# Kernel tuning notes

Hardware: AMD Instinct MI355X
Metric: run time of the kernel (lower is better)

Reference implementation:

```python
import jax, jax.numpy as jnp
import numpy as np

N = 100000      # nodes
E = 1600000     # directed edges (avg degree 16)
F_IN = 128
HID = 64
OUT = 10


def setup_inputs() -> dict:
    key = jax.random.key(0)
    ks = jax.random.split(key, 6)
    x = jax.random.normal(ks[0], (N, F_IN), dtype=jnp.float32)
    edge_index = jax.random.randint(ks[1], (2, E), 0, N, dtype=jnp.int32)
    # Glorot-scaled weights like PyG's GCNConv.lin; bias added post-aggregation
    W1 = jax.random.normal(ks[2], (F_IN, HID), dtype=jnp.float32) * np.float32(1.0 / np.sqrt(F_IN))
    b1 = jnp.zeros((HID,), dtype=jnp.float32)
    W2 = jax.random.normal(ks[3], (HID, OUT), dtype=jnp.float32) * np.float32(1.0 / np.sqrt(HID))
    b2 = jnp.zeros((OUT,), dtype=jnp.float32)
    return {"x": x, "edge_index": edge_index, "W1": W1, "b1": b1, "W2": W2, "b2": b2}


def _gcn_norm(edge_index, num_nodes):
    """Add self-loops and compute symmetric normalization D^-1/2 A D^-1/2 (PyG gcn_norm)."""
    loops = jnp.arange(num_nodes, dtype=edge_index.dtype)
    src = jnp.concatenate([edge_index[0], loops])
    dst = jnp.concatenate([edge_index[1], loops])
    deg = jax.ops.segment_sum(jnp.ones_like(dst, dtype=jnp.float32), dst, num_segments=num_nodes)
    dinv = jnp.where(deg > 0, jax.lax.rsqrt(deg), 0.0)  # inf -> 0 as in PyG
    norm = dinv[src] * dinv[dst]  # [E+N]
    return src, dst, norm


def _gcn_conv(x, src, dst, norm, W, b, num_nodes):
    h = x @ W                                   # transform first (smaller dim aggregated)
    msg = h[src] * norm[:, None]                # gather + scale
    agg = jax.ops.segment_sum(msg, dst, num_segments=num_nodes)  # scatter-add
    return agg + b


def reference(x, edge_index, W1, b1, W2, b2):
    src, dst, norm = _gcn_norm(edge_index, N)
    h = jax.nn.relu(_gcn_conv(x, src, dst, norm, W1, b1, N))
    # F.dropout(training=self.training): identity in eval mode
    out = _gcn_conv(h, src, dst, norm, W2, b2, N)
    return out
```

## Files before the change

### kernel.cpp

```cpp
#include <hip/hip_runtime.h>
#include <hip/hip_fp16.h>

static constexpr int F = 128;
static constexpr int H = 64;
static constexpr int O = 10;
static constexpr int PSU = 6;
static constexpr int NBUK_MAX = 256;
static constexpr int CAP = 12288;
static constexpr int ESCAP = 14336;
static constexpr int EPB = 4096;
static constexpr int XPAD = 136;

typedef _Float16 half8 __attribute__((ext_vector_type(8)));
typedef float floatx4 __attribute__((ext_vector_type(4)));

__global__ __launch_bounds__(256) void k_init(int* __restrict__ bcntg,
                                              const float* __restrict__ W1,
                                              __half* __restrict__ W1f,
                                              unsigned* __restrict__ yN,
                                              unsigned* __restrict__ zsN) {
    int b = blockIdx.x, t = threadIdx.x;
    if (b == 0) {
        bcntg[t] = 0;
        if (t < 32) yN[t] = 0u;
        if (t < PSU) zsN[t] = 0u;
    } else {
        int i = (b - 1) * 256 + t;
        int j = i & 7, lane = (i >> 3) & 63, sc = i >> 9;
        int s = sc >> 2, c = sc & 3;
        int k = s * 32 + (lane >> 4) * 8 + j;
        int nn = c * 16 + (lane & 15);
        W1f[i] = __float2half(W1[k * H + nn]);
    }
}

__global__ __launch_bounds__(256) void k_bin(const int* __restrict__ src,
                                             const int* __restrict__ dst,
                                             int* __restrict__ bcntg,
                                             unsigned* __restrict__ ebuf, int e_total) {
    __shared__ int hist[NBUK_MAX];
    __shared__ int base[NBUK_MAX];
    __shared__ int loc[NBUK_MAX];
    int t = threadIdx.x;
    hist[t] = 0;
    loc[t] = 0;
    __syncthreads();
    int i0 = blockIdx.x * EPB;
    int i1 = min(i0 + EPB, e_total);
    int i = i0 + 4 * t;
    for (; i + 3 < i1; i += 1024) {
        int4 d4 = *(const int4*)&dst[i];
        atomicAdd(&hist[d4.x >> 9], 1);
        atomicAdd(&hist[d4.y >> 9], 1);
        atomicAdd(&hist[d4.z >> 9], 1);
        atomicAdd(&hist[d4.w >> 9], 1);
    }
    for (; i < i1; ++i) atomicAdd(&hist[dst[i] >> 9], 1);
    __syncthreads();
    if (hist[t] > 0) base[t] = atomicAdd(&bcntg[t], hist[t]);
    __syncthreads();
    i = i0 + 4 * t;
    for (; i + 3 < i1; i += 1024) {
        int4 s4 = *(const int4*)&src[i];
        int4 d4 = *(const int4*)&dst[i];
#pragma unroll
        for (int u = 0; u < 4; ++u) {
            int s = (&s4.x)[u], d = (&d4.x)[u];
            int b = d >> 9;
            int r = base[b] + atomicAdd(&loc[b], 1);
            if (r < CAP)
                ebuf[(size_t)b * CAP + r] = ((unsigned)(d & 511) << 17) | (unsigned)s;
        }
    }
    for (; i < i1; ++i) {
        int s = src[i], d = dst[i];
        int b = d >> 9;
        int r = base[b] + atomicAdd(&loc[b], 1);
        if (r < CAP)
            ebuf[(size_t)b * CAP + r] = ((unsigned)(d & 511) << 17) | (unsigned)s;
    }
}

__global__ __launch_bounds__(256) void k_bsort(
    const unsigned* __restrict__ ebuf, const int* __restrict__ bcntg,
    int* __restrict__ rowbeg, int* __restrict__ degp, float* __restrict__ dinv,
    int* __restrict__ esrc, int n_nodes) {
    __shared__ int hc[512];
    __shared__ int sa[512];
    __shared__ int sb[512];
    int t = threadIdx.x, b = blockIdx.x, n0 = b << 9;
    hc[t] = 0;
    hc[t + 256] = 0;
    __syncthreads();
    int cb = min(bcntg[b], CAP);
    const unsigned* eb = ebuf + (size_t)b * CAP;
    int i = 4 * t;
    for (; i + 3 < cb; i += 1024) {
        uint4 e4 = *(const uint4*)&eb[i];
        atomicAdd(&hc[e4.x >> 17], 1);
        atomicAdd(&hc[e4.y >> 17], 1);
        atomicAdd(&hc[e4.z >> 17], 1);
        atomicAdd(&hc[e4.w >> 17], 1);
    }
    for (; i < cb; ++i) atomicAdd(&hc[eb[i] >> 17], 1);
    __syncthreads();
#pragma unroll
    for (int u = 0; u < 2; ++u) {
        int ii = t + 256 * u;
        sa[ii] = (hc[ii] + 7) & ~7;
    }
    __syncthreads();
    int* A = sa;
    int* Bp = sb;
    for (int off = 1; off < 512; off <<= 1) {
#pragma unroll
        for (int u = 0; u < 2; ++u) {
            int ii = t + 256 * u;
            int v = A[ii];
            if (ii >= off) v += A[ii - off];
            Bp[ii] = v;
        }
        __syncthreads();
        int* tmp = A; A = Bp; Bp = tmp;
    }
#pragma unroll
    for (int u = 0; u < 2; ++u) {
        int ii = t + 256 * u;
        int cnt = hc[ii];
        int cp = (cnt + 7) & ~7;
        int excl = A[ii] - cp;
        Bp[ii] = excl;
        int n = n0 + ii;
        if (n < n_nodes) {
            rowbeg[n] = b * ESCAP + excl;
            degp[n] = cp;
            dinv[n] = rsqrtf((float)cnt + 1.0f);
        }
    }
    __syncthreads();
    int* es = esrc + (size_t)b * ESCAP;
    i = 4 * t;
    for (; i + 3 < cb; i += 1024) {
        uint4 e4 = *(const uint4*)&eb[i];
#pragma unroll
        for (int u = 0; u < 4; ++u) {
            unsigned e = (&e4.x)[u];
            int r = atomicAdd(&Bp[e >> 17], 1);
            es[r] = (int)(e & 0x1FFFFu);
        }
    }
    for (; i < cb; ++i) {
        unsigned e = eb[i];
        int r = atomicAdd(&Bp[e >> 17], 1);
        es[r] = (int)(e & 0x1FFFFu);
    }
    __syncthreads();
#pragma unroll
    for (int u = 0; u < 2; ++u) {
        int ii = t + 256 * u;
        int end = A[ii];
        for (int p = Bp[ii]; p < end; ++p) es[p] = n_nodes;
    }
}

__global__ __launch_bounds__(256, 4) void k_gemm1(
    const float* __restrict__ x, const __half* __restrict__ W1f,
    const float* __restrict__ dinv, __half* __restrict__ y, int n_nodes) {
    __shared__ __half xh[64 * XPAD];
    const int tid = threadIdx.x;
    const int lane = tid & 63;
    const int w = tid >> 6;
    const int row0 = blockIdx.x * 64;

    half8 bf[16];
    const uint4* wf = (const uint4*)W1f;
#pragma unroll
    for (int sc = 0; sc < 16; ++sc) {
        union { uint4 u; half8 h; } tmp;
        tmp.u = wf[sc * 64 + lane];
        bf[sc] = tmp.h;
    }

    for (int i = tid; i < 64 * 32; i += 256) {
        int r = i >> 5, k4 = i & 31;
        int gr = row0 + r;
        if (gr < n_nodes) {
            float4 v = *(const float4*)&x[(size_t)gr * F + 4 * k4];
            __half2 p0 = __floats2half2_rn(v.x, v.y);
            __half2 p1 = __floats2half2_rn(v.z, v.w);
            uint2 pk = make_uint2(*(unsigned*)&p0, *(unsigned*)&p1);
            *(uint2*)&xh[r * XPAD + 4 * k4] = pk;
        }
    }
    __syncthreads();

    const int m16 = lane & 15, quad = lane >> 4;
    floatx4 acc[4];
#pragma unroll
    for (int c = 0; c < 4; ++c) acc[c] = (floatx4){0.f, 0.f, 0.f, 0.f};
#pragma unroll
    for (int s = 0; s < 4; ++s) {
        union { uint4 u; half8 h; } ua;
        ua.u = *(const uint4*)&xh[(16 * w + m16) * XPAD + s * 32 + quad * 8];
#pragma unroll
        for (int c = 0; c < 4; ++c)
            acc[c] = __builtin_amdgcn_mfma_f32_16x16x32_f16(ua.h, bf[s * 4 + c],
                                                            acc[c], 0, 0, 0);
    }
#pragma unroll
    for (int r = 0; r < 4; ++r) {
        int grow = row0 + 16 * w + quad * 4 + r;
        if (grow < n_nodes) {
            float d = dinv[grow];
#pragma unroll
            for (int c = 0; c < 4; ++c)
                y[(size_t)grow * H + c * 16 + m16] = __float2half(acc[c][r] * d);
        }
    }
}

__global__ __launch_bounds__(256) void k_gather1z(
    const uint4* __restrict__ yq4, const int* __restrict__ rowbeg,
    const int* __restrict__ degp, const int* __restrict__ esrc,
    const float* __restrict__ dinv, const float* __restrict__ b1,
    const float* __restrict__ W2, unsigned* __restrict__ zs_u, int n_nodes) {
    __shared__ float w2t[O * H];
    for (int i = threadIdx.x; i < O * H; i += 256)
        w2t[i] = W2[(i & 63) * O + (i >> 6)];
    __syncthreads();
    const int l = threadIdx.x & 63;
    const int c = l & 7;
    const int gbase = l & ~7;
    const int n = blockIdx.x * 32 + (threadIdx.x >> 3);
    if (n >= n_nodes) return;
    const int beg = rowbeg[n];
    const int dp = degp[n];
    const float d = dinv[n];

    float acc[8];
    {
        uint4 v = yq4[(size_t)n * 8 + c];
        float2 f0 = __half22float2(*(const __half2*)&v.x);
        float2 f1 = __half22float2(*(const __half2*)&v.y);
        float2 f2 = __half22float2(*(const __half2*)&v.z);
        float2 f3 = __half22float2(*(const __half2*)&v.w);
        acc[0] = f0.x; acc[1] = f0.y; acc[2] = f1.x; acc[3] = f1.y;
        acc[4] = f2.x; acc[5] = f2.y; acc[6] = f3.x; acc[7] = f3.y;
    }
    for (int k0 = 0; k0 < dp; k0 += 8) {
        int idx = esrc[beg + k0 + c];
#pragma unroll
        for (int e = 0; e < 8; ++e) {
            int s = __shfl(idx, gbase + e, 64);
            uint4 v = yq4[(size_t)s * 8 + c];
            float2 f0 = __half22float2(*(const __half2*)&v.x);
            float2 f1 = __half22float2(*(const __half2*)&v.y);
            float2 f2 = __half22float2(*(const __half2*)&v.z);
            float2 f3 = __half22float2(*(const __half2*)&v.w);
            acc[0] += f0.x; acc[1] += f0.y; acc[2] += f1.x; acc[3] += f1.y;
            acc[4] += f2.x; acc[5] += f2.y; acc[6] += f3.x; acc[7] += f3.y;
        }
    }
    const float4 ba = ((const float4*)b1)[2 * c];
    const float4 bbv = ((const float4*)b1)[2 * c + 1];
    float h[8];
    h[0] = fmaxf(fmaf(d, acc[0], ba.x), 0.0f);
    h[1] = fmaxf(fmaf(d, acc[1], ba.y), 0.0f);
    h[2] = fmaxf(fmaf(d, acc[2], ba.z), 0.0f);
    h[3] = fmaxf(fmaf(d, acc[3], ba.w), 0.0f);
    h[4] = fmaxf(fmaf(d, acc[4], bbv.x), 0.0f);
    h[5] = fmaxf(fmaf(d, acc[5], bbv.y), 0.0f);
    h[6] = fmaxf(fmaf(d, acc[6], bbv.z), 0.0f);
    h[7] = fmaxf(fmaf(d, acc[7], bbv.w), 0.0f);
    float p[O];
#pragma unroll
    for (int j = 0; j < O; ++j) {
        float4 wa = *(const float4*)&w2t[j * 64 + 8 * c];
        float4 wb = *(const float4*)&w2t[j * 64 + 8 * c + 4];
        p[j] = h[0] * wa.x + h[1] * wa.y + h[2] * wa.z + h[3] * wa.w
             + h[4] * wb.x + h[5] * wb.y + h[6] * wb.z + h[7] * wb.w;
    }
#pragma unroll
    for (int m = 1; m <= 4; m <<= 1) {
#pragma unroll
        for (int j = 0; j < O; ++j) p[j] += __shfl_xor(p[j], m, 64);
    }
    if (c == 0) {
        __half2 q0 = __floats2half2_rn(p[0] * d, p[1] * d);
        __half2 q1 = __floats2half2_rn(p[2] * d, p[3] * d);
        __half2 q2 = __floats2half2_rn(p[4] * d, p[5] * d);
        __half2 q3 = __floats2half2_rn(p[6] * d, p[7] * d);
        __half2 q4 = __floats2half2_rn(p[8] * d, p[9] * d);
        uint2* zp = (uint2*)&zs_u[(size_t)n * PSU];
        zp[0] = make_uint2(*(const unsigned*)&q0, *(const unsigned*)&q1);
        zp[1] = make_uint2(*(const unsigned*)&q2, *(const unsigned*)&q3);
        zp[2] = make_uint2(*(const unsigned*)&q4, 0u);
    }
}

__global__ __launch_bounds__(256) void k_gather2(
    const unsigned* __restrict__ zs_u, const int* __restrict__ rowbeg,
    const int* __restrict__ degp, const int* __restrict__ esrc,
    const float* __restrict__ dinv, const float* __restrict__ b2,
    float* __restrict__ out, int n_nodes) {
    const int l = threadIdx.x & 63;
    const int j = l & 3;
    const int gb = l & ~3;
    const int jj = (j < 3) ? j : 2;
    const int n = blockIdx.x * 64 + (threadIdx.x >> 2);
    if (n >= n_nodes) return;
    const int beg = rowbeg[n];
    const int dp = degp[n];
    uint2 v0 = *(const uint2*)&zs_u[(size_t)n * PSU + 2 * jj];
    float2 accA = __half22float2(*(const __half2*)&v0.x);
    float2 accB = __half22float2(*(const __half2*)&v0.y);
    for (int k0 = 0; k0 < dp; k0 += 8) {
        int2 idx = *(const int2*)&esrc[beg + k0 + 2 * j];
#pragma unroll
        for (int e = 0; e < 8; ++e) {
            int s = __shfl((e & 1) ? idx.y : idx.x, gb + (e >> 1), 64);
            uint2 v = *(const uint2*)&zs_u[(size_t)s * PSU + 2 * jj];
            float2 fA = __half22float2(*(const __half2*)&v.x);
            float2 fB = __half22float2(*(const __half2*)&v.y);
            accA.x += fA.x; accA.y += fA.y;
            accB.x += fB.x; accB.y += fB.y;
        }
    }
    if (j < 3) {
        const float d = dinv[n];
        float2 bbA = ((const float2*)b2)[2 * j];
        float2 oA = make_float2(fmaf(d, accA.x, bbA.x), fmaf(d, accA.y, bbA.y));
        *(float2*)&out[(size_t)n * O + 4 * j] = oA;
        if (j < 2) {
            float2 bbB = ((const float2*)b2)[2 * j + 1];
            float2 oB = make_float2(fmaf(d, accB.x, bbB.x), fmaf(d, accB.y, bbB.y));
            *(float2*)&out[(size_t)n * O + 4 * j + 2] = oB;
        }
    }
}

static inline size_t align256(size_t v) { return (v + 255) & ~(size_t)255; }

extern "C" void kernel_launch(void* const* d_in, const int* in_sizes, int n_in,
                              void* d_out, int out_size, void* d_ws, size_t ws_size,
                              hipStream_t stream) {
    const float* x  = (const float*)d_in[0];
    const int*   ei = (const int*)d_in[1];
    const float* W1 = (const float*)d_in[2];
    const float* b1 = (const float*)d_in[3];
    const float* W2 = (const float*)d_in[4];
    const float* b2 = (const float*)d_in[5];
    float* out = (float*)d_out;

    const int N = in_sizes[0] / F;
    const int E = in_sizes[1] / 2;
    const int* src = ei;
    const int* dst = ei + E;
    const int NBUK = (N + 511) >> 9;

    char* base = (char*)d_ws;
    __half* y = (__half*)base;
    size_t ysz = align256((size_t)(N + 1) * H * 2);
    char* hreg = base + ysz;
    unsigned* ebuf = (unsigned*)hreg;
    __half* W1f = (__half*)(hreg + (size_t)N * H * 2 - (size_t)F * H * 2);
    size_t hsz = align256((size_t)N * H * 2);
    char* zreg = hreg + hsz;
    unsigned* zs_u = (unsigned*)zreg;
    size_t zsz = align256((size_t)(N + 1) * PSU * 4);
    float* dinv = (float*)(zreg + zsz);
    int* rowbeg = (int*)(dinv + N);
    int* degp = rowbeg + N;
    int* bcntg = degp + N;
    int* esrc = bcntg + 256;

    const int nb_bin = (E + EPB - 1) / EPB;

    k_init<<<1 + F * H / 256, 256, 0, stream>>>(bcntg, W1, W1f,
                                                (unsigned*)(y + (size_t)N * H),
                                                zs_u + (size_t)N * PSU);
    k_bin<<<nb_bin, 256, 0, stream>>>(src, dst, bcntg, ebuf, E);
    k_bsort<<<NBUK, 256, 0, stream>>>(ebuf, bcntg, rowbeg, degp, dinv, esrc, N);
    k_gemm1<<<(N + 63) / 64, 256, 0, stream>>>(x, W1f, dinv, y, N);
    k_gather1z<<<(N + 31) / 32, 256, 0, stream>>>((const uint4*)y, rowbeg, degp,
                                                  esrc, dinv, b1, W2, zs_u, N);
    k_gather2<<<(N + 63) / 64, 256, 0, stream>>>(zs_u, rowbeg, degp, esrc,
                                                 dinv, b2, out, N);
}
```

Baseline: 189.7 us.

## Replace bucket sort CSR build with global degree atomics and fuse scatter into GEMM launch

The two-pass bucketed CSR construction (bin into per-bucket buffers, then a per-bucket local sort) is replaced with a global-atomic degree count, a per-bucket scan that writes row starts and cursors, and a scatter pass using global atomics on per-node cursors. The scatter blocks are merged into the same launch as the first GEMM, so edge scattering and the feature transform can run concurrently and one launch plus the intermediate ebuf traffic go away. In exchange, every edge now does a global atomic to a random node address, which may contend more than the previous LDS atomics. Edge order within each row also becomes nondeterministic.

```diff
diff --git a/kernel.cpp b/kernel.cpp
--- a/kernel.cpp
+++ b/kernel.cpp
@@ -5,8 +5,6 @@
 static constexpr int H = 64;
 static constexpr int O = 10;
 static constexpr int PSU = 6;
-static constexpr int NBUK_MAX = 256;
-static constexpr int CAP = 12288;
 static constexpr int ESCAP = 14336;
 static constexpr int EPB = 4096;
 static constexpr int XPAD = 136;
@@ -14,18 +12,21 @@
 typedef _Float16 half8 __attribute__((ext_vector_type(8)));
 typedef float floatx4 __attribute__((ext_vector_type(4)));
 
-__global__ __launch_bounds__(256) void k_init(int* __restrict__ bcntg,
+__global__ __launch_bounds__(256) void k_init(int* __restrict__ deg,
                                               const float* __restrict__ W1,
                                               __half* __restrict__ W1f,
                                               unsigned* __restrict__ yN,
-                                              unsigned* __restrict__ zsN) {
+                                              unsigned* __restrict__ zsN,
+                                              int n_nodes) {
     int b = blockIdx.x, t = threadIdx.x;
-    if (b == 0) {
-        bcntg[t] = 0;
+    if (b < 391) {
+        int i = b * 256 + t;
+        if (i < n_nodes) deg[i] = 0;
+    } else if (b == 391) {
         if (t < 32) yN[t] = 0u;
         if (t < PSU) zsN[t] = 0u;
     } else {
-        int i = (b - 1) * 256 + t;
+        int i = (b - 392) * 256 + t;
         int j = i & 7, lane = (i >> 3) & 63, sc = i >> 9;
         int s = sc >> 2, c = sc & 3;
         int k = s * 32 + (lane >> 4) * 8 + j;
@@ -34,80 +35,36 @@
     }
 }
 
-__global__ __launch_bounds__(256) void k_bin(const int* __restrict__ src,
-                                             const int* __restrict__ dst,
-                                             int* __restrict__ bcntg,
-                                             unsigned* __restrict__ ebuf, int e_total) {
-    __shared__ int hist[NBUK_MAX];
-    __shared__ int base[NBUK_MAX];
-    __shared__ int loc[NBUK_MAX];
-    int t = threadIdx.x;
-    hist[t] = 0;
-    loc[t] = 0;
-    __syncthreads();
-    int i0 = blockIdx.x * EPB;
-    int i1 = min(i0 + EPB, e_total);
-    int i = i0 + 4 * t;
-    for (; i + 3 < i1; i += 1024) {
+__global__ __launch_bounds__(256) void k_deg(const int* __restrict__ dst,
+                                             int* __restrict__ deg, int e_total) {
+    int i = (blockIdx.x * 256 + threadIdx.x) * 4;
+    if (i + 3 < e_total) {
         int4 d4 = *(const int4*)&dst[i];
-        atomicAdd(&hist[d4.x >> 9], 1);
-        atomicAdd(&hist[d4.y >> 9], 1);
-        atomicAdd(&hist[d4.z >> 9], 1);
-        atomicAdd(&hist[d4.w >> 9], 1);
-    }
-    for (; i < i1; ++i) atomicAdd(&hist[dst[i] >> 9], 1);
-    __syncthreads();
-    if (hist[t] > 0) base[t] = atomicAdd(&bcntg[t], hist[t]);
-    __syncthreads();
-    i = i0 + 4 * t;
-    for (; i + 3 < i1; i += 1024) {
-        int4 s4 = *(const int4*)&src[i];
-        int4 d4 = *(const int4*)&dst[i];
-#pragma unroll
-        for (int u = 0; u < 4; ++u) {
-            int s = (&s4.x)[u], d = (&d4.x)[u];
-            int b = d >> 9;
-            int r = base[b] + atomicAdd(&loc[b], 1);
-            if (r < CAP)
-                ebuf[(size_t)b * CAP + r] = ((unsigned)(d & 511) << 17) | (unsigned)s;
-        }
-    }
-    for (; i < i1; ++i) {
-        int s = src[i], d = dst[i];
-        int b = d >> 9;
-        int r = base[b] + atomicAdd(&loc[b], 1);
-        if (r < CAP)
-            ebuf[(size_t)b * CAP + r] = ((unsigned)(d & 511) << 17) | (unsigned)s;
-    }
-}
-
-__global__ __launch_bounds__(256) void k_bsort(
-    const unsigned* __restrict__ ebuf, const int* __restrict__ bcntg,
-    int* __restrict__ rowbeg, int* __restrict__ degp, float* __restrict__ dinv,
-    int* __restrict__ esrc, int n_nodes) {
-    __shared__ int hc[512];
+        atomicAdd(&deg[d4.x], 1);
+        atomicAdd(&deg[d4.y], 1);
+        atomicAdd(&deg[d4.z], 1);
+        atomicAdd(&deg[d4.w], 1);
+    } else {
+        for (; i < e_total; ++i) atomicAdd(&deg[dst[i]], 1);
+    }
+}
+
+__global__ __launch_bounds__(256) void k_scan(
+    const int* __restrict__ deg, int* __restrict__ rowbeg, int* __restrict__ degp,
+    float* __restrict__ dinv, int* __restrict__ wcur, int* __restrict__ esrc,
+    int n_nodes) {
     __shared__ int sa[512];
     __shared__ int sb[512];
     int t = threadIdx.x, b = blockIdx.x, n0 = b << 9;
-    hc[t] = 0;
-    hc[t + 256] = 0;
-    __syncthreads();
-    int cb = min(bcntg[b], CAP);
-    const unsigned* eb = ebuf + (size_t)b * CAP;
-    int i = 4 * t;
-    for (; i + 3 < cb; i += 1024) {
-        uint4 e4 = *(const uint4*)&eb[i];
-        atomicAdd(&hc[e4.x >> 17], 1);
-        atomicAdd(&hc[e4.y >> 17], 1);
-        atomicAdd(&hc[e4.z >> 17], 1);
-        atomicAdd(&hc[e4.w >> 17], 1);
-    }
-    for (; i < cb; ++i) atomicAdd(&hc[eb[i] >> 17], 1);
-    __syncthreads();
+    int cnt[2], cp[2];
 #pragma unroll
     for (int u = 0; u < 2; ++u) {
         int ii = t + 256 * u;
-        sa[ii] = (hc[ii] + 7) & ~7;
+        int n = n0 + ii;
+        int c = (n < n_nodes) ? deg[n] : 0;
+        cnt[u] = c;
+        cp[u] = (c + 7) & ~7;
+        sa[ii] = cp[u];
     }
     __syncthreads();
     int* A = sa;
@@ -126,51 +83,51 @@
 #pragma unroll
     for (int u = 0; u < 2; ++u) {
         int ii = t + 256 * u;
-        int cnt = hc[ii];
-        int cp = (cnt + 7) & ~7;
-        int excl = A[ii] - cp;
-        Bp[ii] = excl;
         int n = n0 + ii;
         if (n < n_nodes) {
-            rowbeg[n] = b * ESCAP + excl;
-            degp[n] = cp;
-            dinv[n] = rsqrtf((float)cnt + 1.0f);
-        }
-    }
-    __syncthreads();
-    int* es = esrc + (size_t)b * ESCAP;
-    i = 4 * t;
-    for (; i + 3 < cb; i += 1024) {
-        uint4 e4 = *(const uint4*)&eb[i];
-#pragma unroll
-        for (int u = 0; u < 4; ++u) {
-            unsigned e = (&e4.x)[u];
-            int r = atomicAdd(&Bp[e >> 17], 1);
-            es[r] = (int)(e & 0x1FFFFu);
-        }
-    }
-    for (; i < cb; ++i) {
-        unsigned e = eb[i];
-        int r = atomicAdd(&Bp[e >> 17], 1);
-        es[r] = (int)(e & 0x1FFFFu);
-    }
-    __syncthreads();
-#pragma unroll
-    for (int u = 0; u < 2; ++u) {
-        int ii = t + 256 * u;
-        int end = A[ii];
-        for (int p = Bp[ii]; p < end; ++p) es[p] = n_nodes;
-    }
-}
-
-__global__ __launch_bounds__(256, 4) void k_gemm1(
+            int excl = A[ii] - cp[u];
+            int beg = b * ESCAP + excl;
+            rowbeg[n] = beg;
+            degp[n] = cp[u];
+            dinv[n] = rsqrtf((float)cnt[u] + 1.0f);
+            wcur[n] = beg;
+            for (int p = beg + cnt[u]; p < beg + cp[u]; ++p)
+                esrc[p] = n_nodes;
+        }
+    }
+}
+
+__global__ __launch_bounds__(256, 4) void k_scatter_gemm(
+    const int* __restrict__ src, const int* __restrict__ dst,
+    int* __restrict__ wcur, int* __restrict__ esrc,
     const float* __restrict__ x, const __half* __restrict__ W1f,
-    const float* __restrict__ dinv, __half* __restrict__ y, int n_nodes) {
+    const float* __restrict__ dinv, __half* __restrict__ y,
+    int n_nodes, int e_total, int nb_sc) {
     __shared__ __half xh[64 * XPAD];
     const int tid = threadIdx.x;
+    if ((int)blockIdx.x < nb_sc) {
+        int i0 = blockIdx.x * EPB;
+        int i1 = min(i0 + EPB, e_total);
+        int i = i0 + 4 * tid;
+        for (; i + 3 < i1; i += 1024) {
+            int4 s4 = *(const int4*)&src[i];
+            int4 d4 = *(const int4*)&dst[i];
+#pragma unroll
+            for (int u = 0; u < 4; ++u) {
+                int s = (&s4.x)[u], d = (&d4.x)[u];
+                int r = atomicAdd(&wcur[d], 1);
+                esrc[r] = s;
+            }
+        }
+        for (; i < i1; ++i) {
+            int r = atomicAdd(&wcur[dst[i]], 1);
+            esrc[r] = src[i];
+        }
+        return;
+    }
     const int lane = tid & 63;
     const int w = tid >> 6;
-    const int row0 = blockIdx.x * 64;
+    const int row0 = ((int)blockIdx.x - nb_sc) * 64;
 
     half8 bf[16];
     const uint4* wf = (const uint4*)W1f;
@@ -362,7 +319,8 @@
     __half* y = (__half*)base;
     size_t ysz = align256((size_t)(N + 1) * H * 2);
     char* hreg = base + ysz;
-    unsigned* ebuf = (unsigned*)hreg;
+    int* deg = (int*)hreg;
+    int* wcur = deg + N;
     __half* W1f = (__half*)(hreg + (size_t)N * H * 2 - (size_t)F * H * 2);
     size_t hsz = align256((size_t)N * H * 2);
     char* zreg = hreg + hsz;
@@ -371,17 +329,18 @@
     float* dinv = (float*)(zreg + zsz);
     int* rowbeg = (int*)(dinv + N);
     int* degp = rowbeg + N;
-    int* bcntg = degp + N;
-    int* esrc = bcntg + 256;
-
-    const int nb_bin = (E + EPB - 1) / EPB;
-
-    k_init<<<1 + F * H / 256, 256, 0, stream>>>(bcntg, W1, W1f,
-                                                (unsigned*)(y + (size_t)N * H),
-                                                zs_u + (size_t)N * PSU);
-    k_bin<<<nb_bin, 256, 0, stream>>>(src, dst, bcntg, ebuf, E);
-    k_bsort<<<NBUK, 256, 0, stream>>>(ebuf, bcntg, rowbeg, degp, dinv, esrc, N);
-    k_gemm1<<<(N + 63) / 64, 256, 0, stream>>>(x, W1f, dinv, y, N);
+    int* esrc = degp + N;
+
+    const int NB_SC = (E + EPB - 1) / EPB;
+    const int NB_GM = (N + 63) / 64;
+
+    k_init<<<392 + F * H / 256, 256, 0, stream>>>(deg, W1, W1f,
+                                                  (unsigned*)(y + (size_t)N * H),
+                                                  zs_u + (size_t)N * PSU, N);
+    k_deg<<<(E + 1023) / 1024, 256, 0, stream>>>(dst, deg, E);
+    k_scan<<<NBUK, 256, 0, stream>>>(deg, rowbeg, degp, dinv, wcur, esrc, N);
+    k_scatter_gemm<<<NB_SC + NB_GM, 256, 0, stream>>>(src, dst, wcur, esrc,
+                                                      x, W1f, dinv, y, N, E, NB_SC);
     k_gather1z<<<(N + 31) / 32, 256, 0, stream>>>((const uint4*)y, rowbeg, degp,
                                                   esrc, dinv, b1, W2, zs_u, N);
     k_gather2<<<(N + 63) / 64, 256, 0, stream>>>(zs_u, rowbeg, degp, esrc,
```

Measured after the change: 299.3 us. 57.7% more time.

## Compute degrees in binning pass and fuse bucket sort with layer-1 GEMM

Applied to the files above, without the earlier changes.

Per-node in-degree is now counted with global atomics during the binning kernel, so the bucket-sort kernel no longer rebuilds a per-bucket histogram from the edge buffer. The bucket sort and the first GEMM become one launch that splits work by block index, and the GEMM computes its normalization from the degree array directly. This removes one kernel launch and the dependency of the GEMM on the sort, letting them overlap. In exchange it adds 1.6M global atomics in k_bin and a zeroing pass in k_init with a hardcoded block count of 391.

```diff
diff --git a/kernel.cpp b/kernel.cpp
--- a/kernel.cpp
+++ b/kernel.cpp
@@ -14,18 +14,23 @@
 typedef _Float16 half8 __attribute__((ext_vector_type(8)));
 typedef float floatx4 __attribute__((ext_vector_type(4)));
 
-__global__ __launch_bounds__(256) void k_init(int* __restrict__ bcntg,
+__global__ __launch_bounds__(256) void k_init(int* __restrict__ deg,
+                                              int* __restrict__ bcntg,
                                               const float* __restrict__ W1,
                                               __half* __restrict__ W1f,
                                               unsigned* __restrict__ yN,
-                                              unsigned* __restrict__ zsN) {
+                                              unsigned* __restrict__ zsN,
+                                              int n_nodes) {
     int b = blockIdx.x, t = threadIdx.x;
-    if (b == 0) {
+    if (b < 391) {
+        int i = b * 256 + t;
+        if (i < n_nodes) deg[i] = 0;
+    } else if (b == 391) {
         bcntg[t] = 0;
         if (t < 32) yN[t] = 0u;
         if (t < PSU) zsN[t] = 0u;
     } else {
-        int i = (b - 1) * 256 + t;
+        int i = (b - 392) * 256 + t;
         int j = i & 7, lane = (i >> 3) & 63, sc = i >> 9;
         int s = sc >> 2, c = sc & 3;
         int k = s * 32 + (lane >> 4) * 8 + j;
@@ -37,6 +42,7 @@
 __global__ __launch_bounds__(256) void k_bin(const int* __restrict__ src,
                                              const int* __restrict__ dst,
                                              int* __restrict__ bcntg,
+                                             int* __restrict__ deg,
                                              unsigned* __restrict__ ebuf, int e_total) {
     __shared__ int hist[NBUK_MAX];
     __shared__ int base[NBUK_MAX];
@@ -54,8 +60,16 @@
         atomicAdd(&hist[d4.y >> 9], 1);
         atomicAdd(&hist[d4.z >> 9], 1);
         atomicAdd(&hist[d4.w >> 9], 1);
-    }
-    for (; i < i1; ++i) atomicAdd(&hist[dst[i] >> 9], 1);
+        atomicAdd(&deg[d4.x], 1);
+        atomicAdd(&deg[d4.y], 1);
+        atomicAdd(&deg[d4.z], 1);
+        atomicAdd(&deg[d4.w], 1);
+    }
+    for (; i < i1; ++i) {
+        int d = dst[i];
+        atomicAdd(&hist[d >> 9], 1);
+        atomicAdd(&deg[d], 1);
+    }
     __syncthreads();
     if (hist[t] > 0) base[t] = atomicAdd(&bcntg[t], hist[t]);
     __syncthreads();
@@ -81,96 +95,85 @@
     }
 }
 
-__global__ __launch_bounds__(256) void k_bsort(
+__global__ __launch_bounds__(256, 4) void k_bsg(
     const unsigned* __restrict__ ebuf, const int* __restrict__ bcntg,
-    int* __restrict__ rowbeg, int* __restrict__ degp, float* __restrict__ dinv,
-    int* __restrict__ esrc, int n_nodes) {
-    __shared__ int hc[512];
+    const int* __restrict__ deg, int* __restrict__ rowbeg, int* __restrict__ degp,
+    float* __restrict__ dinv, int* __restrict__ esrc,
+    const float* __restrict__ x, const __half* __restrict__ W1f,
+    __half* __restrict__ y, int n_nodes, int nb_bs) {
+    __shared__ __half xh[64 * XPAD];
     __shared__ int sa[512];
     __shared__ int sb[512];
-    int t = threadIdx.x, b = blockIdx.x, n0 = b << 9;
-    hc[t] = 0;
-    hc[t + 256] = 0;
-    __syncthreads();
-    int cb = min(bcntg[b], CAP);
-    const unsigned* eb = ebuf + (size_t)b * CAP;
-    int i = 4 * t;
-    for (; i + 3 < cb; i += 1024) {
-        uint4 e4 = *(const uint4*)&eb[i];
-        atomicAdd(&hc[e4.x >> 17], 1);
-        atomicAdd(&hc[e4.y >> 17], 1);
-        atomicAdd(&hc[e4.z >> 17], 1);
-        atomicAdd(&hc[e4.w >> 17], 1);
-    }
-    for (; i < cb; ++i) atomicAdd(&hc[eb[i] >> 17], 1);
-    __syncthreads();
-#pragma unroll
-    for (int u = 0; u < 2; ++u) {
-        int ii = t + 256 * u;
-        sa[ii] = (hc[ii] + 7) & ~7;
-    }
-    __syncthreads();
-    int* A = sa;
-    int* Bp = sb;
-    for (int off = 1; off < 512; off <<= 1) {
+    const int tid = threadIdx.x;
+    if ((int)blockIdx.x < nb_bs) {
+        const int b = blockIdx.x, n0 = b << 9;
+        int cnt[2], cp[2];
 #pragma unroll
         for (int u = 0; u < 2; ++u) {
-            int ii = t + 256 * u;
-            int v = A[ii];
-            if (ii >= off) v += A[ii - off];
-            Bp[ii] = v;
+            int ii = tid + 256 * u;
+            int n = n0 + ii;
+            int c = (n < n_nodes) ? deg[n] : 0;
+            cnt[u] = c;
+            cp[u] = (c + 7) & ~7;
+            sa[ii] = cp[u];
         }
         __syncthreads();
-        int* tmp = A; A = Bp; Bp = tmp;
-    }
-#pragma unroll
-    for (int u = 0; u < 2; ++u) {
-        int ii = t + 256 * u;
-        int cnt = hc[ii];
-        int cp = (cnt + 7) & ~7;
-        int excl = A[ii] - cp;
-        Bp[ii] = excl;
-        int n = n0 + ii;
-        if (n < n_nodes) {
-            rowbeg[n] = b * ESCAP + excl;
-            degp[n] = cp;
-            dinv[n] = rsqrtf((float)cnt + 1.0f);
-        }
-    }
-    __syncthreads();
-    int* es = esrc + (size_t)b * ESCAP;
-    i = 4 * t;
-    for (; i + 3 < cb; i += 1024) {
-        uint4 e4 = *(const uint4*)&eb[i];
-#pragma unroll
-        for (int u = 0; u < 4; ++u) {
-            unsigned e = (&e4.x)[u];
+        int* A = sa;
+        int* Bp = sb;
+        for (int off = 1; off < 512; off <<= 1) {
+#pragma unroll
+            for (int u = 0; u < 2; ++u) {
+                int ii = tid + 256 * u;
+                int v = A[ii];
+                if (ii >= off) v += A[ii - off];
+                Bp[ii] = v;
+            }
+            __syncthreads();
+            int* tmp = A; A = Bp; Bp = tmp;
+        }
+#pragma unroll
+        for (int u = 0; u < 2; ++u) {
+            int ii = tid + 256 * u;
+            int excl = A[ii] - cp[u];
+            Bp[ii] = excl;
+            int n = n0 + ii;
+            if (n < n_nodes) {
+                rowbeg[n] = b * ESCAP + excl;
+                degp[n] = cp[u];
+                dinv[n] = rsqrtf((float)cnt[u] + 1.0f);
+            }
+        }
+        __syncthreads();
+        const int cb = min(bcntg[b], CAP);
+        const unsigned* eb = ebuf + (size_t)b * CAP;
+        int* es = esrc + (size_t)b * ESCAP;
+        int i = 4 * tid;
+        for (; i + 3 < cb; i += 1024) {
+            uint4 e4 = *(const uint4*)&eb[i];
+#pragma unroll
+            for (int u = 0; u < 4; ++u) {
+                unsigned e = (&e4.x)[u];
+                int r = atomicAdd(&Bp[e >> 17], 1);
+                es[r] = (int)(e & 0x1FFFFu);
+            }
+        }
+        for (; i < cb; ++i) {
+            unsigned e = eb[i];
             int r = atomicAdd(&Bp[e >> 17], 1);
             es[r] = (int)(e & 0x1FFFFu);
         }
-    }
-    for (; i < cb; ++i) {
-        unsigned e = eb[i];
-        int r = atomicAdd(&Bp[e >> 17], 1);
-        es[r] = (int)(e & 0x1FFFFu);
-    }
-    __syncthreads();
-#pragma unroll
-    for (int u = 0; u < 2; ++u) {
-        int ii = t + 256 * u;
-        int end = A[ii];
-        for (int p = Bp[ii]; p < end; ++p) es[p] = n_nodes;
-    }
-}
-
-__global__ __launch_bounds__(256, 4) void k_gemm1(
-    const float* __restrict__ x, const __half* __restrict__ W1f,
-    const float* __restrict__ dinv, __half* __restrict__ y, int n_nodes) {
-    __shared__ __half xh[64 * XPAD];
-    const int tid = threadIdx.x;
+        __syncthreads();
+#pragma unroll
+        for (int u = 0; u < 2; ++u) {
+            int ii = tid + 256 * u;
+            int end = A[ii];
+            for (int p = Bp[ii]; p < end; ++p) es[p] = n_nodes;
+        }
+        return;
+    }
     const int lane = tid & 63;
     const int w = tid >> 6;
-    const int row0 = blockIdx.x * 64;
+    const int row0 = ((int)blockIdx.x - nb_bs) * 64;
 
     half8 bf[16];
     const uint4* wf = (const uint4*)W1f;
@@ -211,7 +214,7 @@
     for (int r = 0; r < 4; ++r) {
         int grow = row0 + 16 * w + quad * 4 + r;
         if (grow < n_nodes) {
-            float d = dinv[grow];
+            float d = rsqrtf((float)deg[grow] + 1.0f);
 #pragma unroll
             for (int c = 0; c < 4; ++c)
                 y[(size_t)grow * H + c * 16 + m16] = __float2half(acc[c][r] * d);
@@ -363,6 +366,7 @@
     size_t ysz = align256((size_t)(N + 1) * H * 2);
     char* hreg = base + ysz;
     unsigned* ebuf = (unsigned*)hreg;
+    int* deg = (int*)(hreg + (size_t)NBUK * CAP * 4);
     __half* W1f = (__half*)(hreg + (size_t)N * H * 2 - (size_t)F * H * 2);
     size_t hsz = align256((size_t)N * H * 2);
     char* zreg = hreg + hsz;
@@ -375,13 +379,14 @@
     int* esrc = bcntg + 256;
 
     const int nb_bin = (E + EPB - 1) / EPB;
-
-    k_init<<<1 + F * H / 256, 256, 0, stream>>>(bcntg, W1, W1f,
-                                                (unsigned*)(y + (size_t)N * H),
-                                                zs_u + (size_t)N * PSU);
-    k_bin<<<nb_bin, 256, 0, stream>>>(src, dst, bcntg, ebuf, E);
-    k_bsort<<<NBUK, 256, 0, stream>>>(ebuf, bcntg, rowbeg, degp, dinv, esrc, N);
-    k_gemm1<<<(N + 63) / 64, 256, 0, stream>>>(x, W1f, dinv, y, N);
+    const int NB_GM = (N + 63) / 64;
+
+    k_init<<<392 + F * H / 256, 256, 0, stream>>>(deg, bcntg, W1, W1f,
+                                                  (unsigned*)(y + (size_t)N * H),
+                                                  zs_u + (size_t)N * PSU, N);
+    k_bin<<<nb_bin, 256, 0, stream>>>(src, dst, bcntg, deg, ebuf, E);
+    k_bsg<<<NBUK + NB_GM, 256, 0, stream>>>(ebuf, bcntg, deg, rowbeg, degp,
+                                            dinv, esrc, x, W1f, y, N, NBUK);
     k_gather1z<<<(N + 31) / 32, 256, 0, stream>>>((const uint4*)y, rowbeg, degp,
                                                   esrc, dinv, b1, W2, zs_u, N);
     k_gather2<<<(N + 63) / 64, 256, 0, stream>>>(zs_u, rowbeg, degp, esrc,
```

Result: slower. 245.2 us (+29.2%).

## Fuse edge binning and first GEMM into one launch; move source dinv into gather

Applied to the files above, without the earlier changes.

The edge-binning kernel and the first-layer GEMM are merged into one horizontally fused launch: the first blocks bin edges and the rest run the GEMM. This works because the GEMM no longer scales rows by dinv. The source-side normalization is now applied in the layer-1 gather, which loads dinv per neighbour chunk, shuffles it across the group and uses FMA. A sentinel dinv entry for padding indices is zeroed. The aim is to save one launch and overlap the atomic-heavy binning with the bandwidth-bound GEMM, at the cost of extra dinv loads in the gather.

```diff
diff --git a/kernel.cpp b/kernel.cpp
--- a/kernel.cpp
+++ b/kernel.cpp
@@ -34,50 +34,103 @@
     }
 }
 
-__global__ __launch_bounds__(256) void k_bin(const int* __restrict__ src,
-                                             const int* __restrict__ dst,
-                                             int* __restrict__ bcntg,
-                                             unsigned* __restrict__ ebuf, int e_total) {
+__global__ __launch_bounds__(256, 4) void k_bingemm(
+    const int* __restrict__ src, const int* __restrict__ dst,
+    int* __restrict__ bcntg, unsigned* __restrict__ ebuf, int e_total,
+    const float* __restrict__ x, const __half* __restrict__ W1f,
+    __half* __restrict__ y, int n_nodes, int nb_bin) {
+    __shared__ __half xh[64 * XPAD];
     __shared__ int hist[NBUK_MAX];
     __shared__ int base[NBUK_MAX];
     __shared__ int loc[NBUK_MAX];
-    int t = threadIdx.x;
-    hist[t] = 0;
-    loc[t] = 0;
-    __syncthreads();
-    int i0 = blockIdx.x * EPB;
-    int i1 = min(i0 + EPB, e_total);
-    int i = i0 + 4 * t;
-    for (; i + 3 < i1; i += 1024) {
-        int4 d4 = *(const int4*)&dst[i];
-        atomicAdd(&hist[d4.x >> 9], 1);
-        atomicAdd(&hist[d4.y >> 9], 1);
-        atomicAdd(&hist[d4.z >> 9], 1);
-        atomicAdd(&hist[d4.w >> 9], 1);
-    }
-    for (; i < i1; ++i) atomicAdd(&hist[dst[i] >> 9], 1);
-    __syncthreads();
-    if (hist[t] > 0) base[t] = atomicAdd(&bcntg[t], hist[t]);
-    __syncthreads();
-    i = i0 + 4 * t;
-    for (; i + 3 < i1; i += 1024) {
-        int4 s4 = *(const int4*)&src[i];
-        int4 d4 = *(const int4*)&dst[i];
-#pragma unroll
-        for (int u = 0; u < 4; ++u) {
-            int s = (&s4.x)[u], d = (&d4.x)[u];
+    const int t = threadIdx.x;
+    if ((int)blockIdx.x < nb_bin) {
+        hist[t] = 0;
+        loc[t] = 0;
+        __syncthreads();
+        int i0 = blockIdx.x * EPB;
+        int i1 = min(i0 + EPB, e_total);
+        int i = i0 + 4 * t;
+        for (; i + 3 < i1; i += 1024) {
+            int4 d4 = *(const int4*)&dst[i];
+            atomicAdd(&hist[d4.x >> 9], 1);
+            atomicAdd(&hist[d4.y >> 9], 1);
+            atomicAdd(&hist[d4.z >> 9], 1);
+            atomicAdd(&hist[d4.w >> 9], 1);
+        }
+        for (; i < i1; ++i) atomicAdd(&hist[dst[i] >> 9], 1);
+        __syncthreads();
+        if (hist[t] > 0) base[t] = atomicAdd(&bcntg[t], hist[t]);
+        __syncthreads();
+        i = i0 + 4 * t;
+        for (; i + 3 < i1; i += 1024) {
+            int4 s4 = *(const int4*)&src[i];
+            int4 d4 = *(const int4*)&dst[i];
+#pragma unroll
+            for (int u = 0; u < 4; ++u) {
+                int s = (&s4.x)[u], d = (&d4.x)[u];
+                int b = d >> 9;
+                int r = base[b] + atomicAdd(&loc[b], 1);
+                if (r < CAP)
+                    ebuf[(size_t)b * CAP + r] = ((unsigned)(d & 511) << 17) | (unsigned)s;
+            }
+        }
+        for (; i < i1; ++i) {
+            int s = src[i], d = dst[i];
             int b = d >> 9;
             int r = base[b] + atomicAdd(&loc[b], 1);
             if (r < CAP)
                 ebuf[(size_t)b * CAP + r] = ((unsigned)(d & 511) << 17) | (unsigned)s;
         }
-    }
-    for (; i < i1; ++i) {
-        int s = src[i], d = dst[i];
-        int b = d >> 9;
-        int r = base[b] + atomicAdd(&loc[b], 1);
-        if (r < CAP)
-            ebuf[(size_t)b * CAP + r] = ((unsigned)(d & 511) << 17) | (unsigned)s;
+        return;
+    }
+    const int lane = t & 63;
+    const int w = t >> 6;
+    const int row0 = ((int)blockIdx.x - nb_bin) * 64;
+
+    half8 bf[16];
+    const uint4* wf = (const uint4*)W1f;
+#pragma unroll
+    for (int sc = 0; sc < 16; ++sc) {
+        union { uint4 u; half8 h; } tmp;
+        tmp.u = wf[sc * 64 + lane];
+        bf[sc] = tmp.h;
+    }
+
+    for (int i = t; i < 64 * 32; i += 256) {
+        int r = i >> 5, k4 = i & 31;
+        int gr = row0 + r;
+        if (gr < n_nodes) {
+            float4 v = *(const float4*)&x[(size_t)gr * F + 4 * k4];
+            __half2 p0 = __floats2half2_rn(v.x, v.y);
+            __half2 p1 = __floats2half2_rn(v.z, v.w);
+            uint2 pk = make_uint2(*(unsigned*)&p0, *(unsigned*)&p1);
+            *(uint2*)&xh[r * XPAD + 4 * k4] = pk;
+        }
+    }
+    __syncthreads();
+
+    const int m16 = lane & 15, quad = lane >> 4;
+    floatx4 acc[4];
+#pragma unroll
+    for (int c = 0; c < 4; ++c) acc[c] = (floatx4){0.f, 0.f, 0.f, 0.f};
+#pragma unroll
+    for (int s = 0; s < 4; ++s) {
+        union { uint4 u; half8 h; } ua;
+        ua.u = *(const uint4*)&xh[(16 * w + m16) * XPAD + s * 32 + quad * 8];
+#pragma unroll
+        for (int c = 0; c < 4; ++c)
+            acc[c] = __builtin_amdgcn_mfma_f32_16x16x32_f16(ua.h, bf[s * 4 + c],
+                                                            acc[c], 0, 0, 0);
+    }
+#pragma unroll
+    for (int r = 0; r < 4; ++r) {
+        int grow = row0 + 16 * w + quad * 4 + r;
+        if (grow < n_nodes) {
+#pragma unroll
+            for (int c = 0; c < 4; ++c)
+                y[(size_t)grow * H + c * 16 + m16] = __float2half(acc[c][r]);
+        }
     }
 }
 
@@ -89,6 +142,7 @@
     __shared__ int sa[512];
     __shared__ int sb[512];
     int t = threadIdx.x, b = blockIdx.x, n0 = b << 9;
+    if (b == 0 && t == 0) dinv[n_nodes] = 0.0f;
     hc[t] = 0;
     hc[t + 256] = 0;
     __syncthreads();
@@ -163,62 +217,6 @@
     }
 }
 
-__global__ __launch_bounds__(256, 4) void k_gemm1(
-    const float* __restrict__ x, const __half* __restrict__ W1f,
-    const float* __restrict__ dinv, __half* __restrict__ y, int n_nodes) {
-    __shared__ __half xh[64 * XPAD];
-    const int tid = threadIdx.x;
-    const int lane = tid & 63;
-    const int w = tid >> 6;
-    const int row0 = blockIdx.x * 64;
-
-    half8 bf[16];
-    const uint4* wf = (const uint4*)W1f;
-#pragma unroll
-    for (int sc = 0; sc < 16; ++sc) {
-        union { uint4 u; half8 h; } tmp;
-        tmp.u = wf[sc * 64 + lane];
-        bf[sc] = tmp.h;
-    }
-
-    for (int i = tid; i < 64 * 32; i += 256) {
-        int r = i >> 5, k4 = i & 31;
-        int gr = row0 + r;
-        if (gr < n_nodes) {
-            float4 v = *(const float4*)&x[(size_t)gr * F + 4 * k4];
-            __half2 p0 = __floats2half2_rn(v.x, v.y);
-            __half2 p1 = __floats2half2_rn(v.z, v.w);
-            uint2 pk = make_uint2(*(unsigned*)&p0, *(unsigned*)&p1);
-            *(uint2*)&xh[r * XPAD + 4 * k4] = pk;
-        }
-    }
-    __syncthreads();
-
-    const int m16 = lane & 15, quad = lane >> 4;
-    floatx4 acc[4];
-#pragma unroll
-    for (int c = 0; c < 4; ++c) acc[c] = (floatx4){0.f, 0.f, 0.f, 0.f};
-#pragma unroll
-    for (int s = 0; s < 4; ++s) {
-        union { uint4 u; half8 h; } ua;
-        ua.u = *(const uint4*)&xh[(16 * w + m16) * XPAD + s * 32 + quad * 8];
-#pragma unroll
-        for (int c = 0; c < 4; ++c)
-            acc[c] = __builtin_amdgcn_mfma_f32_16x16x32_f16(ua.h, bf[s * 4 + c],
-                                                            acc[c], 0, 0, 0);
-    }
-#pragma unroll
-    for (int r = 0; r < 4; ++r) {
-        int grow = row0 + 16 * w + quad * 4 + r;
-        if (grow < n_nodes) {
-            float d = dinv[grow];
-#pragma unroll
-            for (int c = 0; c < 4; ++c)
-                y[(size_t)grow * H + c * 16 + m16] = __float2half(acc[c][r] * d);
-        }
-    }
-}
-
 __global__ __launch_bounds__(256) void k_gather1z(
     const uint4* __restrict__ yq4, const int* __restrict__ rowbeg,
     const int* __restrict__ degp, const int* __restrict__ esrc,
@@ -244,21 +242,25 @@
         float2 f1 = __half22float2(*(const __half2*)&v.y);
         float2 f2 = __half22float2(*(const __half2*)&v.z);
         float2 f3 = __half22float2(*(const __half2*)&v.w);
-        acc[0] = f0.x; acc[1] = f0.y; acc[2] = f1.x; acc[3] = f1.y;
-        acc[4] = f2.x; acc[5] = f2.y; acc[6] = f3.x; acc[7] = f3.y;
+        acc[0] = f0.x * d; acc[1] = f0.y * d; acc[2] = f1.x * d; acc[3] = f1.y * d;
+        acc[4] = f2.x * d; acc[5] = f2.y * d; acc[6] = f3.x * d; acc[7] = f3.y * d;
     }
     for (int k0 = 0; k0 < dp; k0 += 8) {
         int idx = esrc[beg + k0 + c];
+        float dvl = dinv[idx];
 #pragma unroll
         for (int e = 0; e < 8; ++e) {
             int s = __shfl(idx, gbase + e, 64);
+            float dv = __shfl(dvl, gbase + e, 64);
             uint4 v = yq4[(size_t)s * 8 + c];
             float2 f0 = __half22float2(*(const __half2*)&v.x);
             float2 f1 = __half22float2(*(const __half2*)&v.y);
             float2 f2 = __half22float2(*(const __half2*)&v.z);
             float2 f3 = __half22float2(*(const __half2*)&v.w);
-            acc[0] += f0.x; acc[1] += f0.y; acc[2] += f1.x; acc[3] += f1.y;
-            acc[4] += f2.x; acc[5] += f2.y; acc[6] += f3.x; acc[7] += f3.y;
+            acc[0] = fmaf(f0.x, dv, acc[0]); acc[1] = fmaf(f0.y, dv, acc[1]);
+            acc[2] = fmaf(f1.x, dv, acc[2]); acc[3] = fmaf(f1.y, dv, acc[3]);
+            acc[4] = fmaf(f2.x, dv, acc[4]); acc[5] = fmaf(f2.y, dv, acc[5]);
+            acc[6] = fmaf(f3.x, dv, acc[6]); acc[7] = fmaf(f3.y, dv, acc[7]);
         }
     }
     const float4 ba = ((const float4*)b1)[2 * c];
@@ -369,19 +371,20 @@
     unsigned* zs_u = (unsigned*)zreg;
     size_t zsz = align256((size_t)(N + 1) * PSU * 4);
     float* dinv = (float*)(zreg + zsz);
-    int* rowbeg = (int*)(dinv + N);
+    int* rowbeg = (int*)(dinv + N + 1);
     int* degp = rowbeg + N;
     int* bcntg = degp + N;
     int* esrc = bcntg + 256;
 
-    const int nb_bin = (E + EPB - 1) / EPB;
+    const int NB_BIN = (E + EPB - 1) / EPB;
+    const int NB_GM = (N + 63) / 64;
 
     k_init<<<1 + F * H / 256, 256, 0, stream>>>(bcntg, W1, W1f,
                                                 (unsigned*)(y + (size_t)N * H),
                                                 zs_u + (size_t)N * PSU);
-    k_bin<<<nb_bin, 256, 0, stream>>>(src, dst, bcntg, ebuf, E);
+    k_bingemm<<<NB_BIN + NB_GM, 256, 0, stream>>>(src, dst, bcntg, ebuf, E,
+                                                  x, W1f, y, N, NB_BIN);
     k_bsort<<<NBUK, 256, 0, stream>>>(ebuf, bcntg, rowbeg, degp, dinv, esrc, N);
-    k_gemm1<<<(N + 63) / 64, 256, 0, stream>>>(x, W1f, dinv, y, N);
     k_gather1z<<<(N + 31) / 32, 256, 0, stream>>>((const uint4*)y, rowbeg, degp,
                                                   esrc, dinv, b1, W2, zs_u, N);
     k_gather2<<<(N + 63) / 64, 256, 0, stream>>>(zs_u, rowbeg, degp, esrc,
```

After: 193.6 us. 1.02x slower.
